# Optimization experiments

Hardware: AMD Instinct MI355X
Metric: run time of the kernel (lower is better)

## Reference

```python
import jax, jax.numpy as jnp
import numpy as np

B, N, CACHE = 2, 2048, 512
D_MODEL, N_HEADS, HEAD_DIM, FF, KSZ = 768, 12, 64, 3072, 31
EPS = 1e-5


def rmsnorm(x, w):
    return x * jax.lax.rsqrt(jnp.mean(x * x, axis=-1, keepdims=True) + EPS) * w


def rope(x, pos):
    # x: [B, T, H, D], pos: [T] (absolute positions incl. cache offset)
    half = x.shape[-1] // 2
    inv = 1.0 / (10000.0 ** (jnp.arange(half, dtype=jnp.float32) / half))
    ang = pos.astype(jnp.float32)[:, None] * inv[None, :]           # [T, half]
    cos = jnp.concatenate([jnp.cos(ang), jnp.cos(ang)], -1)[None, :, None, :]
    sin = jnp.concatenate([jnp.sin(ang), jnp.sin(ang)], -1)[None, :, None, :]
    x1, x2 = x[..., :half], x[..., half:]
    rot = jnp.concatenate([-x2, x1], -1)
    return x * cos + rot * sin


def setup_inputs() -> dict:
    key = jax.random.key(0)
    ks = jax.random.split(key, 16)
    w = lambda k, shape: jax.random.normal(k, shape, jnp.float32) * 0.02
    kk = jax.random.split(ks[15], 16)
    return {
        "x": jax.random.normal(ks[0], (B, N, D_MODEL), jnp.float32),
        "attn_mask": jnp.ones((B, CACHE + N), bool),
        "pad_mask": jnp.zeros((B, N), bool),
        "length": N,
        "cached_kv": jax.random.normal(ks[1], (B, CACHE, 2, N_HEADS, HEAD_DIM), jnp.float32),
        "ff1_norm_w": jnp.ones((D_MODEL,), jnp.float32),
        "ff1_w1": w(ks[2], (D_MODEL, FF)), "ff1_b1": jnp.zeros((FF,), jnp.float32),
        "ff1_w2": w(ks[3], (FF, D_MODEL)), "ff1_b2": jnp.zeros((D_MODEL,), jnp.float32),
        "attn_norm_w": jnp.ones((D_MODEL,), jnp.float32),
        "qkv_w": w(ks[4], (D_MODEL, 3 * N_HEADS * HEAD_DIM)),
        "out_w": w(ks[5], (N_HEADS * HEAD_DIM, D_MODEL)),
        "q_norm_w": jnp.ones((HEAD_DIM,), jnp.float32),
        "k_norm_w": jnp.ones((HEAD_DIM,), jnp.float32),
        "conv_norm_w": jnp.ones((D_MODEL,), jnp.float32),
        "pw1_w": w(ks[6], (D_MODEL, 2 * D_MODEL)), "pw1_b": jnp.zeros((2 * D_MODEL,), jnp.float32),
        "dw_w": w(ks[7], (D_MODEL, KSZ)), "dw_b": jnp.zeros((D_MODEL,), jnp.float32),
        "bn_g": jnp.ones((D_MODEL,), jnp.float32), "bn_b": jnp.zeros((D_MODEL,), jnp.float32),
        "pw2_w": w(ks[8], (D_MODEL, D_MODEL)), "pw2_b": jnp.zeros((D_MODEL,), jnp.float32),
        "ff2_norm_w": jnp.ones((D_MODEL,), jnp.float32),
        "ff2_w1": w(kk[0], (D_MODEL, FF)), "ff2_b1": jnp.zeros((FF,), jnp.float32),
        "ff2_w2": w(kk[1], (FF, D_MODEL)), "ff2_b2": jnp.zeros((D_MODEL,), jnp.float32),
        "out_norm_w": jnp.ones((D_MODEL,), jnp.float32),
    }


def _ff(x, nw, w1, b1, w2, b2):
    h = jax.nn.gelu(rmsnorm(x, nw) @ w1 + b1)        # FusedMLP: gelu(tanh approx)
    return 0.5 * (h @ w2 + b2)                        # Scale(0.5, ...)


def _attention(x, pad_mask, attn_mask, cached_kv, nw, qkv_w, out_w, qnw, knw):
    y = rmsnorm(x, nw)
    y = jnp.where(pad_mask[..., None], 0.0, y)
    qkv = (y @ qkv_w).reshape(B, N, N_HEADS, HEAD_DIM, 3)  # (h d qkv) layout
    q, k, v = qkv[..., 0], qkv[..., 1], qkv[..., 2]
    q = rmsnorm(q, qnw)
    k = rmsnorm(k, knw)
    k_full = jnp.concatenate([cached_kv[:, :, 0], k], axis=1)  # [B, KV, H, D]
    v_full = jnp.concatenate([cached_kv[:, :, 1], v], axis=1)
    kv_to_cache = jnp.stack([k_full, v_full], axis=2)          # [B, KV, 2, H, D]
    kv_len = k_full.shape[1]
    pos = jnp.arange(kv_len)
    k_rot = rope(k_full, pos)
    q_rot = rope(q, pos[kv_len - N:])
    scale = 1.0 / jnp.sqrt(jnp.asarray(HEAD_DIM, jnp.float32))
    scores = jnp.einsum('bqhd,bkhd->bhqk', q_rot, k_rot) * scale
    scores = jnp.where(attn_mask[:, None, None, :], scores, jnp.finfo(scores.dtype).min)
    attn = jax.nn.softmax(scores, axis=-1)
    out = jnp.einsum('bhqk,bkhd->bqhd', attn, v_full).reshape(B, N, N_HEADS * HEAD_DIM)
    out = jnp.where(pad_mask[..., None], 0.0, out)
    return out @ out_w, kv_to_cache


def _conv(x, pad_mask, nw, pw1_w, pw1_b, dw_w, dw_b, bn_g, bn_b, pw2_w, pw2_b):
    y = rmsnorm(x, nw)
    y = jnp.where(pad_mask[..., None], 0.0, y)
    y = y @ pw1_w + pw1_b                             # pointwise conv1
    a, b = jnp.split(y, 2, axis=-1)
    y = a * jax.nn.sigmoid(b)                          # GLU
    rhs = dw_w.T[:, None, :]                           # [K, 1, C] (WIO, depthwise)
    y = jax.lax.conv_general_dilated(
        y, rhs, (1,), [(KSZ // 2, KSZ // 2)],
        dimension_numbers=('NWC', 'WIO', 'NWC'),
        feature_group_count=D_MODEL) + dw_b
    m = jnp.mean(y, axis=(0, 1))                       # batch(re)norm, train-mode stats
    v = jnp.var(y, axis=(0, 1))
    y = (y - m) * jax.lax.rsqrt(v + EPS) * bn_g + bn_b
    y = y * jax.nn.sigmoid(y)                          # SiLU
    return y @ pw2_w + pw2_b


def reference(x, attn_mask, pad_mask, length, cached_kv,
              ff1_norm_w, ff1_w1, ff1_b1, ff1_w2, ff1_b2,
              attn_norm_w, qkv_w, out_w, q_norm_w, k_norm_w,
              conv_norm_w, pw1_w, pw1_b, dw_w, dw_b, bn_g, bn_b, pw2_w, pw2_b,
              ff2_norm_w, ff2_w1, ff2_b1, ff2_w2, ff2_b2, out_norm_w):
    x = _ff(x, ff1_norm_w, ff1_w1, ff1_b1, ff1_w2, ff1_b2) + x
    attn_out, kv_to_cache = _attention(x, pad_mask, attn_mask, cached_kv,
                                       attn_norm_w, qkv_w, out_w, q_norm_w, k_norm_w)
    x = attn_out + x
    # NOTE: source code has no residual add around the conv block
    x = _conv(x, pad_mask, conv_norm_w, pw1_w, pw1_b, dw_w, dw_b, bn_g, bn_b, pw2_w, pw2_b)
    x = _ff(x, ff2_norm_w, ff2_w1, ff2_b1, ff2_w2, ff2_b2) + x
    x = rmsnorm(x, out_norm_w)
    return x, kv_to_cache
```

## Files before the change

### kernel.cpp

```cpp
#include <hip/hip_runtime.h>
#include <hip/hip_bf16.h>
#include <math.h>

namespace {
constexpr int Bc   = 2;
constexpr int Nn   = 2048;
constexpr int CACHE= 512;
constexpr int KVL  = 2560;
constexpr int DM   = 768;
constexpr int NH   = 12;
constexpr int HD   = 64;
constexpr int FFD  = 3072;
constexpr int RR   = Bc * Nn;
}
#define EPSF 1e-5f

typedef unsigned short u16;
typedef __bf16 bf16x8 __attribute__((ext_vector_type(8)));
typedef float  f32x4  __attribute__((ext_vector_type(4)));
typedef u16    u16x8  __attribute__((ext_vector_type(8)));
typedef u16    u16x4  __attribute__((ext_vector_type(4)));

#define GPTR(p) ((const __attribute__((address_space(1))) void*)(p))
#define LPTR(p) ((__attribute__((address_space(3))) void*)(p))

__device__ __forceinline__ float fast_exp2(float a) {
  float e;
  asm("v_exp_f32 %0, %1" : "=v"(e) : "v"(a));
  return e;
}
__device__ __forceinline__ float fast_rcp(float x) {
  float r;
  asm("v_rcp_f32 %0, %1" : "=v"(r) : "v"(x));
  return r;
}
__device__ __forceinline__ float geluf(float x) {
  const float u = 0.7978845608028654f * x * (1.0f + 0.044715f * x * x);
  const float e = fast_exp2(u * 2.885390081777927f);
  const float t = (e - 1.0f) * fast_rcp(e + 1.0f);
  return 0.5f * x * (1.0f + t);
}
__device__ __forceinline__ float sigmoidf_(float x) {
  const float e = fast_exp2(-x * 1.4426950408889634f);
  return fast_rcp(1.0f + e);
}
__device__ __forceinline__ u16 f2bf(float x) {
  union { float f; unsigned u; } v; v.f = x;
  unsigned r = (v.u + 0x7fffu + ((v.u >> 16) & 1u)) >> 16;
  return (u16)r;
}
__device__ __forceinline__ float bf2f(u16 u) {
  union { unsigned u; float f; } v; v.u = ((unsigned)u) << 16;
  return v.f;
}
__device__ __forceinline__ void rope_sc(float pos, int j, float* s, float* c) {
  const float e = fast_exp2(-(float)j * 0.41524101186092028f);
  const float rev = pos * (e * 0.15915494309189535f);
  const float fr = rev - floorf(rev);
  asm("v_sin_f32 %0, %1" : "=v"(*s) : "v"(fr));
  asm("v_cos_f32 %0, %1" : "=v"(*c) : "v"(fr));
}

template<bool BF>
__global__ __launch_bounds__(256) void k_rmsnorm2(const float* __restrict__ in,
                                                  const float* __restrict__ w,
                                                  void* __restrict__ outv, int D) {
  const int row = blockIdx.x;
  const float* x = in + (size_t)row * D;
  float ss = 0.f;
  for (int i = threadIdx.x; i < D; i += 256) { float v = x[i]; ss = fmaf(v, v, ss); }
  __shared__ float red[5];
#pragma unroll
  for (int off = 32; off > 0; off >>= 1) ss += __shfl_down(ss, off, 64);
  if ((threadIdx.x & 63) == 0) red[threadIdx.x >> 6] = ss;
  __syncthreads();
  if (threadIdx.x == 0) red[4] = red[0] + red[1] + red[2] + red[3];
  __syncthreads();
  const float scale = rsqrtf(red[4] * (1.0f / (float)D) + EPSF);
  for (int i = threadIdx.x; i < D; i += 256) {
    const float v = x[i] * scale * w[i];
    if (BF) ((u16*)outv)[(size_t)row * D + i] = f2bf(v);
    else    ((float*)outv)[(size_t)row * D + i] = v;
  }
}

__global__ __launch_bounds__(256) void k_wt(const float* __restrict__ W,
                                            u16* __restrict__ Wt, int K, int N) {
  __shared__ __align__(16) u16 T[64][72];
  const int nb = blockIdx.x * 64;
  const int kb = blockIdx.y * 64;
#pragma unroll
  for (int p = 0; p < 4; ++p) {
    const int r = p * 16 + (threadIdx.x >> 4);
    const int c = (threadIdx.x & 15) * 4;
    float4 v = *(const float4*)(W + (size_t)(kb + r) * N + nb + c);
    T[c + 0][r] = f2bf(v.x); T[c + 1][r] = f2bf(v.y);
    T[c + 2][r] = f2bf(v.z); T[c + 3][r] = f2bf(v.w);
  }
  __syncthreads();
  const int cc = (threadIdx.x & 7) * 8;
#pragma unroll
  for (int p = 0; p < 2; ++p) {
    const int rr = p * 32 + (threadIdx.x >> 3);
    *(u16x8*)(Wt + (size_t)(nb + rr) * K + kb + cc) = *(const u16x8*)&T[rr][cc];
  }
}

template<int BN, int MODE, bool OUTBF>
__global__ __launch_bounds__(256) void k_gemm_mfma(const u16* __restrict__ A,
                                                   const u16* __restrict__ Wt,
                                                   const float* __restrict__ bias,
                                                   const float* __restrict__ res,
                                                   void* __restrict__ Cv,
                                                   int K, int Nc) {
  constexpr int BM = 128, BK = 64;
  constexpr int CT = BN / 32;
  __shared__ __align__(16) u16 As[BM * BK];
  __shared__ __align__(16) u16 Bs[BN * BK];
  const int lane = threadIdx.x & 63;
  const int w    = threadIdx.x >> 6;
  const int rowBase = blockIdx.y * BM;
  const int colBase = blockIdx.x * BN;
  const int l15 = lane & 15, quad = lane >> 4;
  const int wr = w >> 1, wc = w & 1;
  const int sw = l15 & 7;

  f32x4 acc[4][CT];
#pragma unroll
  for (int i = 0; i < 4; ++i)
#pragma unroll
    for (int j = 0; j < CT; ++j) acc[i][j] = (f32x4){0.f, 0.f, 0.f, 0.f};

  for (int k0 = 0; k0 < K; k0 += BK) {
#pragma unroll
    for (int s = 0; s < 4; ++s) {
      const int cbase = (w * 4 + s) * 64;
      const int c = cbase + lane;
      const int r = c >> 3;
      const int kc = (c & 7) ^ (r & 7);
      __builtin_amdgcn_global_load_lds(
          GPTR(A + (size_t)(rowBase + r) * K + k0 + kc * 8),
          LPTR((char*)As + (size_t)cbase * 16), 16, 0, 0);
    }
#pragma unroll
    for (int s = 0; s < BN / 32; ++s) {
      const int cbase = (w * (BN / 32) + s) * 64;
      const int c = cbase + lane;
      const int r = c >> 3;
      const int kc = (c & 7) ^ (r & 7);
      __builtin_amdgcn_global_load_lds(
          GPTR(Wt + (size_t)(colBase + r) * K + k0 + kc * 8),
          LPTR((char*)Bs + (size_t)cbase * 16), 16, 0, 0);
    }
    __syncthreads();

#pragma unroll
    for (int kk = 0; kk < 2; ++kk) {
      bf16x8 aF[4], bF[CT];
#pragma unroll
      for (int rt = 0; rt < 4; ++rt) {
        const int row = wr * 64 + rt * 16 + l15;
        aF[rt] = *(const bf16x8*)&As[row * BK + (((kk * 4 + quad) ^ sw) * 8)];
      }
#pragma unroll
      for (int ct = 0; ct < CT; ++ct) {
        const int row = wc * (BN / 2) + ct * 16 + l15;
        bF[ct] = *(const bf16x8*)&Bs[row * BK + (((kk * 4 + quad) ^ sw) * 8)];
      }
#pragma unroll
      for (int rt = 0; rt < 4; ++rt)
#pragma unroll
        for (int ct = 0; ct < CT; ++ct)
          acc[rt][ct] = __builtin_amdgcn_mfma_f32_16x16x32_bf16(aF[rt], bF[ct],
                                                                acc[rt][ct], 0, 0, 0);
    }
    __syncthreads();
  }

#pragma unroll
  for (int ct = 0; ct < CT; ++ct) {
    const int col = colBase + wc * (BN / 2) + ct * 16 + l15;
    const float bv = bias ? bias[col] : 0.f;
#pragma unroll
    for (int rt = 0; rt < 4; ++rt) {
#pragma unroll
      for (int r = 0; r < 4; ++r) {
        const int row = rowBase + wr * 64 + rt * 16 + quad * 4 + r;
        float v = acc[rt][ct][r] + bv;
        if (MODE == 1) v = geluf(v);
        else if (MODE == 2) v = 0.5f * v + res[(size_t)row * Nc + col];
        else if (MODE == 3) v = v + res[(size_t)row * Nc + col];
        if (OUTBF) ((u16*)Cv)[(size_t)row * Nc + col] = f2bf(v);
        else       ((float*)Cv)[(size_t)row * Nc + col] = v;
      }
    }
  }
}

__global__ __launch_bounds__(768) void k_qkv_post(const float* __restrict__ qkv,
                                                  const float* __restrict__ qw,
                                                  const float* __restrict__ kw,
                                                  u16* __restrict__ qbf,
                                                  u16* __restrict__ krotbf,
                                                  float* __restrict__ kvout) {
  const int row = blockIdx.x;
  const int b = row >> 11;
  const int n = row & 2047;
  const int h = threadIdx.x >> 6;
  const int d = threadIdx.x & 63;
  const float* src = qkv + (size_t)row * (3 * DM) + h * 192 + d * 3;
  const float q = src[0], k = src[1], v = src[2];
  float sq = q * q, sk = k * k;
#pragma unroll
  for (int off = 32; off > 0; off >>= 1) {
    sq += __shfl_xor(sq, off, 64);
    sk += __shfl_xor(sk, off, 64);
  }
  const float qs = rsqrtf(sq * (1.0f / 64.0f) + EPSF);
  const float ks = rsqrtf(sk * (1.0f / 64.0f) + EPSF);
  const float qn = q * qs * qw[d];
  const float kn = k * ks * kw[d];
  const size_t kvbase = ((size_t)b * KVL + (CACHE + n)) * (2 * DM) + h * 64 + d;
  kvout[kvbase] = kn;
  kvout[kvbase + DM] = v;
  const int j = d & 31;
  float s, c;
  rope_sc((float)(CACHE + n), j, &s, &c);
  const float oq = __shfl_xor(qn, 32, 64);
  const float ok = __shfl_xor(kn, 32, 64);
  const float rq = (d < 32) ? -oq : oq;
  const float rk = (d < 32) ? -ok : ok;
  qbf[((size_t)row * NH + h) * 64 + d] = f2bf((qn * c + rq * s) * 0.18033688011112042f);
  krotbf[((size_t)(b * KVL + CACHE + n) * NH + h) * 64 + d] = f2bf(kn * c + rk * s);
}

__global__ __launch_bounds__(768) void k_cache_prep(const float* __restrict__ cached,
                                                    float* __restrict__ kvout,
                                                    u16* __restrict__ krotbf) {
  const int row = blockIdx.x;
  const int b = row / CACHE, t = row - b * CACHE;
  const int h = threadIdx.x >> 6;
  const int d = threadIdx.x & 63;
  const float k = cached[((size_t)row * 2 + 0) * DM + h * 64 + d];
  const float v = cached[((size_t)row * 2 + 1) * DM + h * 64 + d];
  const size_t kb = ((size_t)b * KVL + t) * (2 * DM) + h * 64 + d;
  kvout[kb] = k;
  kvout[kb + DM] = v;
  const int j = d & 31;
  float s, c;
  rope_sc((float)t, j, &s, &c);
  const float ok = __shfl_xor(k, 32, 64);
  const float rk = (d < 32) ? -ok : ok;
  krotbf[((size_t)(b * KVL + t) * NH + h) * 64 + d] = f2bf(k * c + rk * s);
}

__global__ __launch_bounds__(256) void k_vt(const float* __restrict__ kvout,
                                            u16* __restrict__ vtbf) {
  __shared__ __align__(16) u16 T[64][72];
  const int bh = blockIdx.x / 40;
  const int tb = blockIdx.x % 40;
  const int b = bh / NH, h = bh % NH;
  const int t0 = tb * 64;
  {
    const int tloc = threadIdx.x >> 2;
    const int dg = (threadIdx.x & 3) * 16;
    const float* src = kvout + ((size_t)b * KVL + t0 + tloc) * (2 * DM) + DM + h * 64 + dg;
    float4 v0 = *(const float4*)(src);
    float4 v1 = *(const float4*)(src + 4);
    float4 v2 = *(const float4*)(src + 8);
    float4 v3 = *(const float4*)(src + 12);
    T[dg + 0][tloc] = f2bf(v0.x);  T[dg + 1][tloc] = f2bf(v0.y);
    T[dg + 2][tloc] = f2bf(v0.z);  T[dg + 3][tloc] = f2bf(v0.w);
    T[dg + 4][tloc] = f2bf(v1.x);  T[dg + 5][tloc] = f2bf(v1.y);
    T[dg + 6][tloc] = f2bf(v1.z);  T[dg + 7][tloc] = f2bf(v1.w);
    T[dg + 8][tloc] = f2bf(v2.x);  T[dg + 9][tloc] = f2bf(v2.y);
    T[dg + 10][tloc] = f2bf(v2.z); T[dg + 11][tloc] = f2bf(v2.w);
    T[dg + 12][tloc] = f2bf(v3.x); T[dg + 13][tloc] = f2bf(v3.y);
    T[dg + 14][tloc] = f2bf(v3.z); T[dg + 15][tloc] = f2bf(v3.w);
  }
  __syncthreads();
  const int d = threadIdx.x >> 2;
  const int kg = (threadIdx.x & 3) * 16;
  u16x8 a = *(const u16x8*)&T[d][kg];
  u16x8 b8 = *(const u16x8*)&T[d][kg + 8];
  u16* dst = vtbf + ((size_t)(b * NH + h) * 64 + d) * KVL + t0 + kg;
  *(u16x8*)dst = a;
  *(u16x8*)(dst + 8) = b8;
}

__global__ __launch_bounds__(256) void k_attn2(const u16* __restrict__ qbf,
                                               const u16* __restrict__ krotbf,
                                               const u16* __restrict__ vtbf,
                                               float* __restrict__ Apart,
                                               float* __restrict__ lpart) {
  __shared__ __align__(16) u16 Ks[2][64 * 64];
  __shared__ __align__(16) u16 Vs[2][64 * 64];
  __shared__ __align__(16) u16 Ps[4][16][64];
  const int lane = threadIdx.x & 63;
  const int wid  = threadIdx.x >> 6;
  const int sp   = blockIdx.x & 1;
  const int rest = blockIdx.x >> 1;
  const int qblk = rest & 31;
  const int bh   = rest >> 5;
  const int b = bh / NH, h = bh % NH;
  const int q0 = qblk * 64 + wid * 16;
  const int l15 = lane & 15;
  const int quad = lane >> 4;
  const int sw = l15 & 7;

  const u16* qp = qbf + ((size_t)(b * Nn + q0 + l15) * NH + h) * 64 + quad * 8;
  const bf16x8 bQ0 = *(const bf16x8*)qp;
  const bf16x8 bQ1 = *(const bf16x8*)(qp + 32);
  asm volatile("" :: "v"(*(const f32x4*)&bQ0), "v"(*(const f32x4*)&bQ1));

  f32x4 O[4] = {};
  float l_lane = 0.f;

  const int c0 = (wid * 2 + 0) * 64 + lane;
  const int c1 = (wid * 2 + 1) * 64 + lane;
  const int r0 = c0 >> 3, kc0 = (c0 & 7) ^ (r0 & 7);
  const int r1 = c1 >> 3, kc1 = (c1 & 7) ^ (r1 & 7);
  const u16* kbase = krotbf + ((size_t)b * KVL * NH + h) * 64;
  const u16* vbase = vtbf + ((size_t)(b * NH + h) * 64) * KVL;
  const u16* ksrc0 = kbase + (size_t)r0 * (NH * 64) + kc0 * 8;
  const u16* ksrc1 = kbase + (size_t)r1 * (NH * 64) + kc1 * 8;
  const u16* vsrc0 = vbase + (size_t)r0 * KVL + kc0 * 8;
  const u16* vsrc1 = vbase + (size_t)r1 * KVL + kc1 * 8;
  const size_t kd0 = (size_t)(wid * 2 + 0) * 1024;
  const size_t kd1 = (size_t)(wid * 2 + 1) * 1024;

  auto stage = [&](int buf, int t0) {
    char* kd = (char*)Ks[buf];
    char* vd = (char*)Vs[buf];
    __builtin_amdgcn_global_load_lds(GPTR(ksrc0 + (size_t)t0 * (NH * 64)),
                                     LPTR(kd + kd0), 16, 0, 0);
    __builtin_amdgcn_global_load_lds(GPTR(vsrc0 + t0), LPTR(vd + kd0), 16, 0, 0);
    __builtin_amdgcn_global_load_lds(GPTR(ksrc1 + (size_t)t0 * (NH * 64)),
                                     LPTR(kd + kd1), 16, 0, 0);
    __builtin_amdgcn_global_load_lds(GPTR(vsrc1 + t0), LPTR(vd + kd1), 16, 0, 0);
  };

  const int tbeg = sp * (KVL / 2);
  constexpr int NT = (KVL / 2) / 64;

  stage(0, tbeg);
  for (int i = 0; i < NT; ++i) {
    const int cur = i & 1;
    if (i + 1 < NT) {
      stage(cur ^ 1, tbeg + (i + 1) * 64);
      asm volatile("s_waitcnt vmcnt(4)" ::: "memory");
    } else {
      asm volatile("s_waitcnt vmcnt(0)" ::: "memory");
    }
    __builtin_amdgcn_s_barrier();
    asm volatile("" ::: "memory");
    const u16* ksc = Ks[cur];
    const u16* vsc = Vs[cur];

#pragma unroll
    for (int nt = 0; nt < 4; ++nt) {
      const int krow = nt * 16 + l15;
      const bf16x8 aK0 = *(const bf16x8*)&ksc[krow * 64 + ((quad ^ sw) * 8)];
      const bf16x8 aK1 = *(const bf16x8*)&ksc[krow * 64 + (((4 + quad) ^ sw) * 8)];
      f32x4 cc = {};
      cc = __builtin_amdgcn_mfma_f32_16x16x32_bf16(aK0, bQ0, cc, 0, 0, 0);
      cc = __builtin_amdgcn_mfma_f32_16x16x32_bf16(aK1, bQ1, cc, 0, 0, 0);
      const float p0 = fast_exp2(cc[0]);
      const float p1 = fast_exp2(cc[1]);
      const float p2 = fast_exp2(cc[2]);
      const float p3 = fast_exp2(cc[3]);
      l_lane += (p0 + p1) + (p2 + p3);
      unsigned w0, w1;
      asm("v_cvt_pk_bf16_f32 %0, %1, %2" : "=v"(w0) : "v"(p0), "v"(p1));
      asm("v_cvt_pk_bf16_f32 %0, %1, %2" : "=v"(w1) : "v"(p2), "v"(p3));
      uint2 pk; pk.x = w0; pk.y = w1;
      const int pg = (nt * 2 + (quad >> 1)) ^ sw;
      *(uint2*)&Ps[wid][l15][pg * 8 + (quad & 1) * 4] = pk;
    }
    asm volatile("s_waitcnt lgkmcnt(0)" ::: "memory");

    __builtin_amdgcn_s_setprio(1);
#pragma unroll
    for (int kt = 0; kt < 2; ++kt) {
      const bf16x8 bP = *(const bf16x8*)&Ps[wid][l15][((kt * 4 + quad) ^ sw) * 8];
#pragma unroll
      for (int ot = 0; ot < 4; ++ot) {
        const int vrow = ot * 16 + l15;
        const bf16x8 aV = *(const bf16x8*)&vsc[vrow * 64 + (((kt * 4 + quad) ^ sw) * 8)];
        O[ot] = __builtin_amdgcn_mfma_f32_16x16x32_bf16(aV, bP, O[ot], 0, 0, 0);
      }
    }
    __builtin_amdgcn_s_setprio(0);
    asm volatile("" ::: "memory");
    __builtin_amdgcn_s_barrier();
  }

  l_lane += __shfl_xor(l_lane, 16, 64);
  l_lane += __shfl_xor(l_lane, 32, 64);
  const int sbh = (sp * Bc + b) * NH + h;
  if (quad == 0) lpart[(size_t)sbh * Nn + q0 + l15] = l_lane;
  float* ap = Apart + ((size_t)sbh * 64) * Nn + q0 + l15;
#pragma unroll
  for (int ot = 0; ot < 4; ++ot)
#pragma unroll
    for (int r = 0; r < 4; ++r)
      ap[(size_t)(ot * 16 + quad * 4 + r) * Nn] = O[ot][r];
}

__global__ __launch_bounds__(256) void k_attn_merge(const float* __restrict__ Apart,
                                                    const float* __restrict__ lpart,
                                                    u16* __restrict__ attnout) {
  __shared__ float T[64][65];
  __shared__ float il[64];
  const int qt = blockIdx.x & 31;
  const int bh = blockIdx.x >> 5;
  const int b = bh / NH, h = bh % NH;
  const int q0 = qt * 64;
  const int bh0 = b * NH + h;
  const int bh1 = (Bc + b) * NH + h;
  if (threadIdx.x < 64) {
    const int q = threadIdx.x;
    il[q] = 1.0f / (lpart[(size_t)bh0 * Nn + q0 + q] + lpart[(size_t)bh1 * Nn + q0 + q]);
  }
  const float* a0 = Apart + ((size_t)bh0 * 64) * Nn + q0;
  const float* a1 = Apart + ((size_t)bh1 * 64) * Nn + q0;
#pragma unroll
  for (int p = 0; p < 16; ++p) {
    const int idx = p * 256 + threadIdx.x;
    const int d = idx >> 6, q = idx & 63;
    T[q][d] = a0[(size_t)d * Nn + q] + a1[(size_t)d * Nn + q];
  }
  __syncthreads();
#pragma unroll
  for (int p = 0; p < 16; ++p) {
    const int idx = p * 256 + threadIdx.x;
    const int q = idx >> 6, d = idx & 63;
    attnout[((size_t)(b * Nn + q0 + q)) * DM + h * 64 + d] = f2bf(T[q][d] * il[q]);
  }
}

__global__ __launch_bounds__(256) void k_dwconv2(const u16* __restrict__ pw1,
                                                 const float* __restrict__ w,
                                                 const float* __restrict__ bsd,
                                                 float* __restrict__ out,
                                                 float* __restrict__ stats) {
  __shared__ float S[94][68];
  __shared__ float Wl[31][64];
  const int cb = blockIdx.x * 64;
  const int n0 = blockIdx.y * 64;
  const int b  = blockIdx.z;
  for (int idx = threadIdx.x; idx < 94 * 16; idx += 256) {
    const int r = idx >> 4, cg = (idx & 15) * 4;
    const int n = n0 - 15 + r;
    float4 v = make_float4(0.f, 0.f, 0.f, 0.f);
    if (n >= 0 && n < Nn) {
      const u16* p = pw1 + ((size_t)(b * Nn + n)) * (2 * DM) + cb + cg;
      u16x4 av = *(const u16x4*)(p);
      u16x4 gv = *(const u16x4*)(p + DM);
      v.x = bf2f(av[0]) * sigmoidf_(bf2f(gv[0]));
      v.y = bf2f(av[1]) * sigmoidf_(bf2f(gv[1]));
      v.z = bf2f(av[2]) * sigmoidf_(bf2f(gv[2]));
      v.w = bf2f(av[3]) * sigmoidf_(bf2f(gv[3]));
    }
    *(float4*)&S[r][cg] = v;
  }
  for (int idx = threadIdx.x; idx < 31 * 64; idx += 256) {
    const int c = idx & 63, tap = idx >> 6;
    Wl[tap][c] = w[(size_t)(cb + c) * 31 + tap];
  }
  __syncthreads();

  const int cg  = (threadIdx.x & 15) * 4;
  const int nl0 = threadIdx.x >> 4;
  const float4 b4 = *(const float4*)(bsd + cb + cg);
  float sum[4] = {0.f, 0.f, 0.f, 0.f};
  float sq[4]  = {0.f, 0.f, 0.f, 0.f};
#pragma unroll
  for (int p = 0; p < 4; ++p) {
    const int nl = p * 16 + nl0;
    float a0 = b4.x, a1 = b4.y, a2 = b4.z, a3 = b4.w;
#pragma unroll
    for (int t = 0; t < 31; ++t) {
      const float4 sv = *(const float4*)&S[nl + t][cg];
      const float4 wv = *(const float4*)&Wl[t][cg & 63];
      a0 = fmaf(sv.x, wv.x, a0); a1 = fmaf(sv.y, wv.y, a1);
      a2 = fmaf(sv.z, wv.z, a2); a3 = fmaf(sv.w, wv.w, a3);
    }
    *(float4*)(out + ((size_t)(b * Nn + n0 + nl)) * DM + cb + cg) =
        make_float4(a0, a1, a2, a3);
    sum[0] += a0; sum[1] += a1; sum[2] += a2; sum[3] += a3;
    sq[0] = fmaf(a0, a0, sq[0]); sq[1] = fmaf(a1, a1, sq[1]);
    sq[2] = fmaf(a2, a2, sq[2]); sq[3] = fmaf(a3, a3, sq[3]);
  }
  __syncthreads();
  *(float4*)&S[nl0][cg]      = make_float4(sum[0], sum[1], sum[2], sum[3]);
  *(float4*)&S[16 + nl0][cg] = make_float4(sq[0], sq[1], sq[2], sq[3]);
  __syncthreads();
  if (threadIdx.x < 64) {
    const int c = threadIdx.x;
    float s = 0.f, q = 0.f;
#pragma unroll
    for (int i = 0; i < 16; ++i) { s += S[i][c]; q += S[16 + i][c]; }
    atomicAdd(&stats[cb + c], s);
    atomicAdd(&stats[DM + cb + c], q);
  }
}

__global__ __launch_bounds__(256) void k_zero(float* __restrict__ p, int n) {
  const int i = blockIdx.x * 256 + threadIdx.x;
  if (i < n) p[i] = 0.f;
}

__global__ __launch_bounds__(256) void k_bn_apply(const float* __restrict__ x,
                                                  const float* __restrict__ stats,
                                                  const float* __restrict__ g,
                                                  const float* __restrict__ bb,
                                                  u16* __restrict__ out) {
  const int idx = blockIdx.x * 256 + threadIdx.x;
  const int c = idx % DM;
  const float mean = stats[c] * (1.0f / (float)RR);
  const float var = stats[DM + c] * (1.0f / (float)RR) - mean * mean;
  float y = (x[idx] - mean) * rsqrtf(var + EPSF) * g[c] + bb[c];
  out[idx] = f2bf(y * sigmoidf_(y));
}

extern "C" void kernel_launch(void* const* d_in, const int* in_sizes, int n_in,
                              void* d_out, int out_size, void* d_ws, size_t ws_size,
                              hipStream_t stream) {
  const float* x       = (const float*)d_in[0];
  const float* cached  = (const float*)d_in[4];
  const float* ff1_nw  = (const float*)d_in[5];
  const float* ff1_w1  = (const float*)d_in[6];
  const float* ff1_b1  = (const float*)d_in[7];
  const float* ff1_w2  = (const float*)d_in[8];
  const float* ff1_b2  = (const float*)d_in[9];
  const float* attn_nw = (const float*)d_in[10];
  const float* qkv_w   = (const float*)d_in[11];
  const float* out_w   = (const float*)d_in[12];
  const float* q_nw    = (const float*)d_in[13];
  const float* k_nw    = (const float*)d_in[14];
  const float* conv_nw = (const float*)d_in[15];
  const float* pw1_w   = (const float*)d_in[16];
  const float* pw1_b   = (const float*)d_in[17];
  const float* dw_w    = (const float*)d_in[18];
  const float* dw_b    = (const float*)d_in[19];
  const float* bn_g    = (const float*)d_in[20];
  const float* bn_b    = (const float*)d_in[21];
  const float* pw2_w   = (const float*)d_in[22];
  const float* pw2_b   = (const float*)d_in[23];
  const float* ff2_nw  = (const float*)d_in[24];
  const float* ff2_w1  = (const float*)d_in[25];
  const float* ff2_b1  = (const float*)d_in[26];
  const float* ff2_w2  = (const float*)d_in[27];
  const float* ff2_b2  = (const float*)d_in[28];
  const float* out_nw  = (const float*)d_in[29];

  float* out_x  = (float*)d_out;
  float* out_kv = out_x + (size_t)RR * DM;

  u16* wt_ff1w1 = (u16*)d_ws;
  u16* wt_ff1w2 = wt_ff1w1 + (size_t)3072 * 768;
  u16* wt_qkv   = wt_ff1w2 + (size_t)768 * 3072;
  u16* wt_out   = wt_qkv   + (size_t)2304 * 768;
  u16* wt_pw1   = wt_out   + (size_t)768 * 768;
  u16* wt_pw2   = wt_pw1   + (size_t)1536 * 768;
  u16* wt_ff2w1 = wt_pw2   + (size_t)768 * 768;
  u16* wt_ff2w2 = wt_ff2w1 + (size_t)3072 * 768;
  u16* abuf     = wt_ff2w2 + (size_t)768 * 3072;
  u16* hbuf     = abuf + (size_t)RR * DM;
  float* xA     = (float*)(hbuf + (size_t)RR * FFD);
  float* xB     = xA + (size_t)RR * DM;
  float* qkvbuf = xB + (size_t)RR * DM;
  u16* qbf      = (u16*)(qkvbuf + (size_t)RR * 3 * DM);
  u16* krotbf   = qbf + (size_t)RR * DM;
  u16* vtbf     = krotbf + (size_t)Bc * KVL * DM;
  float* bn_stats = (float*)(vtbf + (size_t)Bc * KVL * DM);
  float* Apart  = (float*)hbuf;
  u16* attnout  = (u16*)qkvbuf;
  float* lpart  = qkvbuf + (size_t)RR * DM;
  float* dwout  = qkvbuf;
  u16* bnout    = (u16*)(qkvbuf + (size_t)RR * DM);

  const dim3 blk(256);
  k_wt<<<dim3(48, 12), blk, 0, stream>>>(ff1_w1, wt_ff1w1, DM, FFD);
  k_wt<<<dim3(12, 48), blk, 0, stream>>>(ff1_w2, wt_ff1w2, FFD, DM);
  k_wt<<<dim3(36, 12), blk, 0, stream>>>(qkv_w, wt_qkv, DM, 3 * DM);
  k_wt<<<dim3(12, 12), blk, 0, stream>>>(out_w, wt_out, DM, DM);
  k_wt<<<dim3(24, 12), blk, 0, stream>>>(pw1_w, wt_pw1, DM, 2 * DM);
  k_wt<<<dim3(12, 12), blk, 0, stream>>>(pw2_w, wt_pw2, DM, DM);
  k_wt<<<dim3(48, 12), blk, 0, stream>>>(ff2_w1, wt_ff2w1, DM, FFD);
  k_wt<<<dim3(12, 48), blk, 0, stream>>>(ff2_w2, wt_ff2w2, FFD, DM);

  k_rmsnorm2<true><<<RR, blk, 0, stream>>>(x, ff1_nw, abuf, DM);
  k_gemm_mfma<128, 1, true><<<dim3(FFD / 128, RR / 128), blk, 0, stream>>>(
      abuf, wt_ff1w1, ff1_b1, nullptr, hbuf, DM, FFD);
  k_gemm_mfma<64, 2, false><<<dim3(DM / 64, RR / 128), blk, 0, stream>>>(
      hbuf, wt_ff1w2, ff1_b2, x, xA, FFD, DM);
  k_rmsnorm2<true><<<RR, blk, 0, stream>>>(xA, attn_nw, abuf, DM);
  k_gemm_mfma<128, 0, false><<<dim3(3 * DM / 128, RR / 128), blk, 0, stream>>>(
      abuf, wt_qkv, nullptr, nullptr, qkvbuf, DM, 3 * DM);
  k_qkv_post<<<RR, 768, 0, stream>>>(qkvbuf, q_nw, k_nw, qbf, krotbf, out_kv);
  k_cache_prep<<<Bc * CACHE, 768, 0, stream>>>(cached, out_kv, krotbf);
  k_vt<<<Bc * NH * (KVL / 64), blk, 0, stream>>>(out_kv, vtbf);
  k_attn2<<<Bc * NH * (Nn / 64) * 2, blk, 0, stream>>>(qbf, krotbf, vtbf, Apart, lpart);
  k_attn_merge<<<Bc * NH * (Nn / 64), blk, 0, stream>>>(Apart, lpart, attnout);
  k_gemm_mfma<64, 3, false><<<dim3(DM / 64, RR / 128), blk, 0, stream>>>(
      attnout, wt_out, nullptr, xA, xB, DM, DM);
  k_rmsnorm2<true><<<RR, blk, 0, stream>>>(xB, conv_nw, abuf, DM);
  k_gemm_mfma<128, 0, true><<<dim3(2 * DM / 128, RR / 128), blk, 0, stream>>>(
      abuf, wt_pw1, pw1_b, nullptr, hbuf, DM, 2 * DM);
  k_zero<<<6, blk, 0, stream>>>(bn_stats, 2 * DM);
  k_dwconv2<<<dim3(DM / 64, Nn / 64, Bc), blk, 0, stream>>>(hbuf, dw_w, dw_b,
                                                            dwout, bn_stats);
  k_bn_apply<<<RR * DM / 256, blk, 0, stream>>>(dwout, bn_stats, bn_g, bn_b, bnout);
  k_gemm_mfma<64, 0, false><<<dim3(DM / 64, RR / 128), blk, 0, stream>>>(
      bnout, wt_pw2, pw2_b, nullptr, xA, DM, DM);
  k_rmsnorm2<true><<<RR, blk, 0, stream>>>(xA, ff2_nw, abuf, DM);
  k_gemm_mfma<128, 1, true><<<dim3(FFD / 128, RR / 128), blk, 0, stream>>>(
      abuf, wt_ff2w1, ff2_b1, nullptr, hbuf, DM, FFD);
  k_gemm_mfma<64, 2, false><<<dim3(DM / 64, RR / 128), blk, 0, stream>>>(
      hbuf, wt_ff2w2, ff2_b2, xA, xB, FFD, DM);
  k_rmsnorm2<false><<<RR, blk, 0, stream>>>(xB, out_nw, out_x, DM);
}
```

Before: 575.6 us.

## Fuse attention split-KV merge into single-pass kernel and swizzle block order for XCDs

The attention kernel no longer splits the KV range in two with a separate merge kernel. Each block now processes the full KV length, normalizes by the row sum, transposes through shared memory and writes bf16 output directly. This removes the fp32 partial-output round trip through global memory and one kernel launch, at the cost of half as many blocks, each running twice as long. Both GEMM and attention also remap block IDs so consecutive tiles are spread round-robin across the eight XCDs, aiming at better L2 locality.

```diff
diff --git a/kernel.cpp b/kernel.cpp
--- a/kernel.cpp
+++ b/kernel.cpp
@@ -119,8 +119,12 @@
   __shared__ __align__(16) u16 Bs[BN * BK];
   const int lane = threadIdx.x & 63;
   const int w    = threadIdx.x >> 6;
-  const int rowBase = blockIdx.y * BM;
-  const int colBase = blockIdx.x * BN;
+  const int gx = gridDim.x;
+  const int nwg = gx * gridDim.y;
+  int bid = blockIdx.y * gx + blockIdx.x;
+  if ((nwg & 7) == 0) bid = (bid & 7) * (nwg >> 3) + (bid >> 3);
+  const int rowBase = (bid / gx) * BM;
+  const int colBase = (bid % gx) * BN;
   const int l15 = lane & 15, quad = lane >> 4;
   const int wr = w >> 1, wc = w & 1;
   const int sw = l15 & 7;
@@ -288,20 +292,20 @@
   *(u16x8*)(dst + 8) = b8;
 }
 
-__global__ __launch_bounds__(256) void k_attn2(const u16* __restrict__ qbf,
+__global__ __launch_bounds__(256) void k_attn3(const u16* __restrict__ qbf,
                                                const u16* __restrict__ krotbf,
                                                const u16* __restrict__ vtbf,
-                                               float* __restrict__ Apart,
-                                               float* __restrict__ lpart) {
-  __shared__ __align__(16) u16 Ks[2][64 * 64];
-  __shared__ __align__(16) u16 Vs[2][64 * 64];
-  __shared__ __align__(16) u16 Ps[4][16][64];
+                                               u16* __restrict__ attnout) {
+  __shared__ __align__(16) char smem[40960];
+  u16* const KsB = (u16*)smem;
+  u16* const VsB = (u16*)(smem + 16384);
+  u16* const PsB = (u16*)(smem + 32768);
   const int lane = threadIdx.x & 63;
   const int wid  = threadIdx.x >> 6;
-  const int sp   = blockIdx.x & 1;
-  const int rest = blockIdx.x >> 1;
-  const int qblk = rest & 31;
-  const int bh   = rest >> 5;
+  const int bid = blockIdx.x;
+  const int swz = (bid & 7) * (768 / 8) + (bid >> 3);
+  const int qblk = swz & 31;
+  const int bh   = swz >> 5;
   const int b = bh / NH, h = bh % NH;
   const int q0 = qblk * 64 + wid * 16;
   const int l15 = lane & 15;
@@ -330,8 +334,8 @@
   const size_t kd1 = (size_t)(wid * 2 + 1) * 1024;
 
   auto stage = [&](int buf, int t0) {
-    char* kd = (char*)Ks[buf];
-    char* vd = (char*)Vs[buf];
+    char* kd = (char*)(KsB + buf * 4096);
+    char* vd = (char*)(VsB + buf * 4096);
     __builtin_amdgcn_global_load_lds(GPTR(ksrc0 + (size_t)t0 * (NH * 64)),
                                      LPTR(kd + kd0), 16, 0, 0);
     __builtin_amdgcn_global_load_lds(GPTR(vsrc0 + t0), LPTR(vd + kd0), 16, 0, 0);
@@ -340,22 +344,21 @@
     __builtin_amdgcn_global_load_lds(GPTR(vsrc1 + t0), LPTR(vd + kd1), 16, 0, 0);
   };
 
-  const int tbeg = sp * (KVL / 2);
-  constexpr int NT = (KVL / 2) / 64;
-
-  stage(0, tbeg);
+  constexpr int NT = KVL / 64;
+  stage(0, 0);
   for (int i = 0; i < NT; ++i) {
     const int cur = i & 1;
     if (i + 1 < NT) {
-      stage(cur ^ 1, tbeg + (i + 1) * 64);
+      stage(cur ^ 1, (i + 1) * 64);
       asm volatile("s_waitcnt vmcnt(4)" ::: "memory");
     } else {
       asm volatile("s_waitcnt vmcnt(0)" ::: "memory");
     }
     __builtin_amdgcn_s_barrier();
     asm volatile("" ::: "memory");
-    const u16* ksc = Ks[cur];
-    const u16* vsc = Vs[cur];
+    const u16* ksc = KsB + cur * 4096;
+    const u16* vsc = VsB + cur * 4096;
+    u16* Pw = PsB + wid * 1024 + l15 * 64;
 
 #pragma unroll
     for (int nt = 0; nt < 4; ++nt) {
@@ -375,14 +378,14 @@
       asm("v_cvt_pk_bf16_f32 %0, %1, %2" : "=v"(w1) : "v"(p2), "v"(p3));
       uint2 pk; pk.x = w0; pk.y = w1;
       const int pg = (nt * 2 + (quad >> 1)) ^ sw;
-      *(uint2*)&Ps[wid][l15][pg * 8 + (quad & 1) * 4] = pk;
+      *(uint2*)&Pw[pg * 8 + (quad & 1) * 4] = pk;
     }
     asm volatile("s_waitcnt lgkmcnt(0)" ::: "memory");
 
     __builtin_amdgcn_s_setprio(1);
 #pragma unroll
     for (int kt = 0; kt < 2; ++kt) {
-      const bf16x8 bP = *(const bf16x8*)&Ps[wid][l15][((kt * 4 + quad) ^ sw) * 8];
+      const bf16x8 bP = *(const bf16x8*)&Pw[((kt * 4 + quad) ^ sw) * 8];
 #pragma unroll
       for (int ot = 0; ot < 4; ++ot) {
         const int vrow = ot * 16 + l15;
@@ -397,46 +400,31 @@
 
   l_lane += __shfl_xor(l_lane, 16, 64);
   l_lane += __shfl_xor(l_lane, 32, 64);
-  const int sbh = (sp * Bc + b) * NH + h;
-  if (quad == 0) lpart[(size_t)sbh * Nn + q0 + l15] = l_lane;
-  float* ap = Apart + ((size_t)sbh * 64) * Nn + q0 + l15;
+  const float il = 1.0f / l_lane;
+  float* const OF  = (float*)smem;
+  float* const ILs = (float*)(smem + 32768);
+  if (quad == 0) ILs[wid * 16 + l15] = il;
+  float* of = OF + (size_t)(wid * 16 + l15) * 68;
 #pragma unroll
   for (int ot = 0; ot < 4; ++ot)
-#pragma unroll
-    for (int r = 0; r < 4; ++r)
-      ap[(size_t)(ot * 16 + quad * 4 + r) * Nn] = O[ot][r];
-}
-
-__global__ __launch_bounds__(256) void k_attn_merge(const float* __restrict__ Apart,
-                                                    const float* __restrict__ lpart,
-                                                    u16* __restrict__ attnout) {
-  __shared__ float T[64][65];
-  __shared__ float il[64];
-  const int qt = blockIdx.x & 31;
-  const int bh = blockIdx.x >> 5;
-  const int b = bh / NH, h = bh % NH;
-  const int q0 = qt * 64;
-  const int bh0 = b * NH + h;
-  const int bh1 = (Bc + b) * NH + h;
-  if (threadIdx.x < 64) {
-    const int q = threadIdx.x;
-    il[q] = 1.0f / (lpart[(size_t)bh0 * Nn + q0 + q] + lpart[(size_t)bh1 * Nn + q0 + q]);
-  }
-  const float* a0 = Apart + ((size_t)bh0 * 64) * Nn + q0;
-  const float* a1 = Apart + ((size_t)bh1 * 64) * Nn + q0;
-#pragma unroll
-  for (int p = 0; p < 16; ++p) {
-    const int idx = p * 256 + threadIdx.x;
-    const int d = idx >> 6, q = idx & 63;
-    T[q][d] = a0[(size_t)d * Nn + q] + a1[(size_t)d * Nn + q];
-  }
-  __syncthreads();
-#pragma unroll
-  for (int p = 0; p < 16; ++p) {
-    const int idx = p * 256 + threadIdx.x;
-    const int q = idx >> 6, d = idx & 63;
-    attnout[((size_t)(b * Nn + q0 + q)) * DM + h * 64 + d] = f2bf(T[q][d] * il[q]);
-  }
+    *(f32x4*)&of[ot * 16 + quad * 4] = O[ot];
+  asm volatile("s_waitcnt lgkmcnt(0)" ::: "memory");
+  const int q  = lane >> 2;
+  const int dg = (lane & 3) * 16;
+  const float sc = ILs[wid * 16 + q];
+  const float* srcp = OF + (size_t)(wid * 16 + q) * 68 + dg;
+  unsigned wv[8];
+#pragma unroll
+  for (int i2 = 0; i2 < 8; ++i2) {
+    const float a0 = srcp[2 * i2] * sc;
+    const float a1 = srcp[2 * i2 + 1] * sc;
+    asm("v_cvt_pk_bf16_f32 %0, %1, %2" : "=v"(wv[i2]) : "v"(a0), "v"(a1));
+  }
+  u16* dst = attnout + ((size_t)(b * Nn + q0 + q)) * DM + h * 64 + dg;
+  uint4 s0; s0.x = wv[0]; s0.y = wv[1]; s0.z = wv[2]; s0.w = wv[3];
+  uint4 s1; s1.x = wv[4]; s1.y = wv[5]; s1.z = wv[6]; s1.w = wv[7];
+  *(uint4*)dst = s0;
+  *(uint4*)(dst + 8) = s1;
 }
 
 __global__ __launch_bounds__(256) void k_dwconv2(const u16* __restrict__ pw1,
@@ -575,9 +563,7 @@
   u16* krotbf   = qbf + (size_t)RR * DM;
   u16* vtbf     = krotbf + (size_t)Bc * KVL * DM;
   float* bn_stats = (float*)(vtbf + (size_t)Bc * KVL * DM);
-  float* Apart  = (float*)hbuf;
   u16* attnout  = (u16*)qkvbuf;
-  float* lpart  = qkvbuf + (size_t)RR * DM;
   float* dwout  = qkvbuf;
   u16* bnout    = (u16*)(qkvbuf + (size_t)RR * DM);
 
@@ -602,8 +588,7 @@
   k_qkv_post<<<RR, 768, 0, stream>>>(qkvbuf, q_nw, k_nw, qbf, krotbf, out_kv);
   k_cache_prep<<<Bc * CACHE, 768, 0, stream>>>(cached, out_kv, krotbf);
   k_vt<<<Bc * NH * (KVL / 64), blk, 0, stream>>>(out_kv, vtbf);
-  k_attn2<<<Bc * NH * (Nn / 64) * 2, blk, 0, stream>>>(qbf, krotbf, vtbf, Apart, lpart);
-  k_attn_merge<<<Bc * NH * (Nn / 64), blk, 0, stream>>>(Apart, lpart, attnout);
+  k_attn3<<<Bc * NH * (Nn / 64), blk, 0, stream>>>(qbf, krotbf, vtbf, attnout);
   k_gemm_mfma<64, 3, false><<<dim3(DM / 64, RR / 128), blk, 0, stream>>>(
       attnout, wt_out, nullptr, xA, xB, DM, DM);
   k_rmsnorm2<true><<<RR, blk, 0, stream>>>(xB, conv_nw, abuf, DM);
```

Result: faster. 547.0 us (-5.0%).
